# Performance work log

Measured on AMD Instinct MI355X. Metric: run time of the kernel, lower is better.

The kernel has to match this reference:

```python
import jax, jax.numpy as jnp
import numpy as np
from jax import lax

B, S, D = 1, 512, 2048
HK, HV, DK, DV, K = 8, 16, 128, 128, 4
R = HV // HK
KEY_DIM = HK * DK
VAL_DIM = HV * DV
CONV_DIM = 2 * KEY_DIM + VAL_DIM
EPS = 1e-6


def setup_inputs() -> dict:
    key = jax.random.key(0)
    ks = jax.random.split(key, 8)
    hidden_states = jax.random.normal(ks[0], (B, S, D), jnp.float32)
    W_qkvz = jax.random.normal(ks[1], (D, 2 * KEY_DIM + 2 * VAL_DIM), jnp.float32) * 0.02
    W_ba = jax.random.normal(ks[2], (D, 2 * HV), jnp.float32) * 0.02
    conv_w = jax.random.normal(ks[3], (CONV_DIM, 1, K), jnp.float32) * 0.2  # depthwise [C,1,K]
    dt_bias = jnp.ones((HV,), jnp.float32)
    A_log = jnp.log(jax.random.uniform(ks[4], (HV,), jnp.float32, 1e-3, 16.0))
    norm_weight = jnp.ones((DV,), jnp.float32)
    W_out = jax.random.normal(ks[5], (VAL_DIM, D), jnp.float32) * 0.02
    return dict(hidden_states=hidden_states, W_qkvz=W_qkvz, W_ba=W_ba, conv_w=conv_w,
                dt_bias=dt_bias, A_log=A_log, norm_weight=norm_weight, W_out=W_out)


def _l2norm(x):
    return x * lax.rsqrt(jnp.sum(x * x, -1, keepdims=True) + EPS)


def reference(hidden_states, W_qkvz, W_ba, conv_w, dt_bias, A_log, norm_weight, W_out):
    # input projections
    qkvz = hidden_states @ W_qkvz              # [B,S,2*key_dim+2*value_dim]
    ba = hidden_states @ W_ba                  # [B,S,2*HV]
    # _rearrange: split per key-head group
    qkvz = qkvz.reshape(B, S, HK, 2 * DK + 2 * R * DV)
    q = qkvz[..., :DK]                                         # [B,S,HK,DK]
    k = qkvz[..., DK:2 * DK]                                   # [B,S,HK,DK]
    v = qkvz[..., 2 * DK:2 * DK + R * DV].reshape(B, S, HV, DV)
    z = qkvz[..., 2 * DK + R * DV:].reshape(B, S, HV, DV)
    ba = ba.reshape(B, S, HK, 2 * R)
    b = ba[..., :R].reshape(B, S, HV)
    a = ba[..., R:].reshape(B, S, HV)
    # fused causal depthwise conv1d + SiLU over concat(q,k,v)
    mixed = jnp.concatenate([q.reshape(B, S, -1), k.reshape(B, S, -1), v.reshape(B, S, -1)], -1)
    mixed = mixed.transpose(0, 2, 1)           # [B,C,S]
    mixed = lax.conv_general_dilated(mixed, conv_w, (1,), [(K - 1, 0)],
                                     feature_group_count=CONV_DIM,
                                     dimension_numbers=('NCH', 'OIH', 'NCH'))
    mixed = jax.nn.silu(mixed).transpose(0, 2, 1)  # [B,S,C]
    q = mixed[..., :KEY_DIM].reshape(B, S, HK, DK)
    k = mixed[..., KEY_DIM:2 * KEY_DIM].reshape(B, S, HK, DK)
    v = mixed[..., 2 * KEY_DIM:].reshape(B, S, HV, DV)
    # gates
    beta = jax.nn.sigmoid(b)                                   # [B,S,HV]
    g = jnp.exp(-jnp.exp(A_log) * jax.nn.softplus(a + dt_bias))  # per-step decay in (0,1)
    q = _l2norm(q) * (DK ** -0.5)
    k = _l2norm(k)
    q = jnp.repeat(q, R, axis=2)               # GQA expand to HV heads
    k = jnp.repeat(k, R, axis=2)
    # gated delta-rule recurrence over sequence (state per batch/head: [DK,DV])
    def step(Sst, inp):
        qt, kt, vt, gt, bt = inp
        Sst = Sst * gt[..., None, None]
        pred = jnp.einsum('bhk,bhkv->bhv', kt, Sst)
        delta = (vt - pred) * bt[..., None]
        Sst = Sst + jnp.einsum('bhk,bhv->bhkv', kt, delta)
        o = jnp.einsum('bhk,bhkv->bhv', qt, Sst)
        return Sst, o
    xs = (q.transpose(1, 0, 2, 3), k.transpose(1, 0, 2, 3), v.transpose(1, 0, 2, 3),
          g.transpose(1, 0, 2), beta.transpose(1, 0, 2))
    S0 = jnp.zeros((B, HV, DK, DV), jnp.float32)
    _, core = lax.scan(step, S0, xs)           # core: [S,B,HV,DV]
    core = core.transpose(1, 0, 2, 3)          # [B,S,HV,DV]
    # gated RMSNorm per value head, gated by silu(z)
    var = jnp.mean(core * core, -1, keepdims=True)
    normed = core * lax.rsqrt(var + EPS) * norm_weight * jax.nn.silu(z)
    return normed.reshape(B, S, VAL_DIM) @ W_out
```

## Files before the change

kernel.cpp:

```cpp
#include <hip/hip_runtime.h>
#include <hip/hip_bf16.h>
#include <math.h>

#define S_  512
#define D_  2048
#define HK_ 8
#define HV_ 16
#define DK_ 128
#define DV_ 128
#define KEY_DIM_ 1024
#define VAL_DIM_ 2048
#define QKVZ_N  6144
#define EPS_ 1e-6f

typedef __attribute__((ext_vector_type(8))) short short8;
typedef __attribute__((ext_vector_type(4))) float f32x4;
typedef unsigned short ushort_t;
typedef unsigned int uint_t;

__device__ __forceinline__ ushort_t f2bf(float x) {
    uint_t u = __float_as_uint(x);
    return (ushort_t)((u + 0x7FFFu + ((u >> 16) & 1u)) >> 16);
}

__device__ __forceinline__ void gl2lds16(const void* g, void* l) {
    __builtin_amdgcn_global_load_lds((const __attribute__((address_space(1))) uint_t*)g,
                                     (__attribute__((address_space(3))) uint_t*)l, 16, 0, 0);
}
__device__ __forceinline__ void gl2lds4(const void* g, void* l) {
    __builtin_amdgcn_global_load_lds((const __attribute__((address_space(1))) uint_t*)g,
                                     (__attribute__((address_space(3))) uint_t*)l, 4, 0, 0);
}

__global__ __launch_bounds__(256) void convert_bf16(const float* __restrict__ X,
                                                    ushort_t* __restrict__ H, int n4) {
    int i = blockIdx.x * blockDim.x + threadIdx.x;
    if (i >= n4) return;
    float4 v = ((const float4*)X)[i];
    ushort4 h;
    h.x = f2bf(v.x); h.y = f2bf(v.y); h.z = f2bf(v.z); h.w = f2bf(v.w);
    ((ushort4*)H)[i] = h;
}

__global__ __launch_bounds__(256) void transpose_convert(const float* __restrict__ W,
                                                         ushort_t* __restrict__ Th,
                                                         int K, int N) {
    __shared__ float tile[64][65];
    const int kb = blockIdx.y * 64, nb = blockIdx.x * 64;
    const int t = threadIdx.x;
#pragma unroll
    for (int i = 0; i < 4; ++i) {
        int r = (t >> 4) + i * 16;
        int c4 = (t & 15) * 4;
        float4 v = *(const float4*)&W[(size_t)(kb + r) * N + nb + c4];
        tile[r][c4 + 0] = v.x; tile[r][c4 + 1] = v.y;
        tile[r][c4 + 2] = v.z; tile[r][c4 + 3] = v.w;
    }
    __syncthreads();
#pragma unroll
    for (int i = 0; i < 4; ++i) {
        int idx = t + 256 * i;
        int n = idx >> 4;
        int k4 = (idx & 15) * 4;
        ushort4 h;
        h.x = f2bf(tile[k4 + 0][n]); h.y = f2bf(tile[k4 + 1][n]);
        h.z = f2bf(tile[k4 + 2][n]); h.w = f2bf(tile[k4 + 3][n]);
        *(ushort4*)&Th[(size_t)(nb + n) * K + kb + k4] = h;
    }
}

template<int BM, int BN, int WR, int WC>
__global__ __launch_bounds__(256) void gemm_bf16(const ushort_t* __restrict__ A,
                                                 const ushort_t* __restrict__ B,
                                                 float* __restrict__ C,
                                                 int M, int N, int K) {
    constexpr int TM = BM / (16 * WR);
    constexpr int TN = BN / (16 * WC);
    constexpr int AI = (BM / 16) * 2;
    constexpr int BI = (BN / 16) * 2;

    __shared__ __align__(16) ushort_t sA[2][2][BM][32];
    __shared__ __align__(16) ushort_t sB[2][2][BN][32];

    const int t = threadIdx.x;
    const int w = t >> 6, lane = t & 63;
    const int wr = w / WC, wc = w % WC;
    const int lm = lane & 15, quad = lane >> 4;
    const int m0 = blockIdx.y * BM, n0 = blockIdx.x * BN;
    const int lrow = lane >> 2;
    const int lch  = (lane & 3) * 8;

    auto stage = [&](int buf, int k0) {
#pragma unroll
        for (int j = w; j < AI; j += 4) {
            int ks = j & 1, r0 = (j >> 1) * 16;
            gl2lds16(&A[(size_t)(m0 + r0 + lrow) * K + k0 + ks * 32 + lch],
                     &sA[buf][ks][r0][0]);
        }
#pragma unroll
        for (int j = w; j < BI; j += 4) {
            int ks = j & 1, r0 = (j >> 1) * 16;
            gl2lds16(&B[(size_t)(n0 + r0 + lrow) * K + k0 + ks * 32 + lch],
                     &sB[buf][ks][r0][0]);
        }
    };

    f32x4 acc[TM][TN] = {};
    stage(0, 0);
    __syncthreads();

    const int NK = K / 64;
    for (int it = 0; it < NK; ++it) {
        int buf = it & 1;
        if (it + 1 < NK) stage(buf ^ 1, (it + 1) * 64);
#pragma unroll
        for (int ks = 0; ks < 2; ++ks) {
            short8 bf[TN];
#pragma unroll
            for (int ni = 0; ni < TN; ++ni)
                bf[ni] = *(const short8*)&sB[buf][ks][wc * (TN * 16) + ni * 16 + lm][quad * 8];
#pragma unroll
            for (int mi = 0; mi < TM; ++mi) {
                short8 af = *(const short8*)&sA[buf][ks][wr * (TM * 16) + mi * 16 + lm][quad * 8];
#pragma unroll
                for (int ni = 0; ni < TN; ++ni)
                    acc[mi][ni] = __builtin_amdgcn_mfma_f32_16x16x32_bf16(af, bf[ni], acc[mi][ni], 0, 0, 0);
            }
        }
        __syncthreads();
    }

#pragma unroll
    for (int mi = 0; mi < TM; ++mi)
#pragma unroll
        for (int ni = 0; ni < TN; ++ni) {
            int row = m0 + wr * TM * 16 + mi * 16 + quad * 4;
            int col = n0 + wc * TN * 16 + ni * 16 + lm;
#pragma unroll
            for (int r = 0; r < 4; ++r)
                C[(size_t)(row + r) * N + col] = acc[mi][ni][r];
        }
}

__global__ __launch_bounds__(256) void ba_kernel(const float* __restrict__ hid,
                                                 const float* __restrict__ Wba,
                                                 float* __restrict__ ba) {
    const int s = blockIdx.x;
    const int j = threadIdx.x & 31;
    const int kg = threadIdx.x >> 5;
    const float* h = hid + (size_t)s * D_;
    float sum = 0.f;
    const int k0 = kg * 256;
#pragma unroll 8
    for (int k = k0; k < k0 + 256; ++k)
        sum = fmaf(h[k], Wba[(size_t)k * 32 + j], sum);
    __shared__ float red[8][32];
    red[kg][j] = sum;
    __syncthreads();
    if (threadIdx.x < 32) {
        float tot = 0.f;
#pragma unroll
        for (int r = 0; r < 8; ++r) tot += red[r][j];
        ba[s * 32 + j] = tot;
    }
}

__global__ __launch_bounds__(128) void conv_kernel(const float* __restrict__ qkvz,
                                                   const float* __restrict__ conv_w,
                                                   float* __restrict__ qc,
                                                   float* __restrict__ kc,
                                                   float* __restrict__ vc) {
    const int s   = blockIdx.x;
    const int grp = blockIdx.y;
    const int d   = threadIdx.x;

    int col, c;
    if (grp < 8) {
        int hk = grp;
        col = hk * 768 + d;
        c   = hk * 128 + d;
    } else if (grp < 16) {
        int hk = grp - 8;
        col = hk * 768 + 128 + d;
        c   = 1024 + (hk * 128 + d);
    } else {
        int hv = grp - 16;
        col = (hv >> 1) * 768 + 256 + (hv & 1) * 128 + d;
        c   = 2048 + (hv * 128 + d);
    }

    const float w0 = conv_w[c * 4 + 0];
    const float w1 = conv_w[c * 4 + 1];
    const float w2 = conv_w[c * 4 + 2];
    const float w3 = conv_w[c * 4 + 3];

    float x = 0.f;
    if (s - 3 >= 0) x += qkvz[(size_t)(s - 3) * QKVZ_N + col] * w0;
    if (s - 2 >= 0) x += qkvz[(size_t)(s - 2) * QKVZ_N + col] * w1;
    if (s - 1 >= 0) x += qkvz[(size_t)(s - 1) * QKVZ_N + col] * w2;
    x += qkvz[(size_t)s * QKVZ_N + col] * w3;

    x = x / (1.f + expf(-x));

    if (grp < 16) {
        float ss = x * x;
#pragma unroll
        for (int m = 1; m < 64; m <<= 1) ss += __shfl_xor(ss, m);
        __shared__ float red[2];
        int wid = threadIdx.x >> 6;
        if ((threadIdx.x & 63) == 0) red[wid] = ss;
        __syncthreads();
        float tot = red[0] + red[1];
        float scale = rsqrtf(tot + EPS_);
        if (grp < 8) {
            x = x * scale * 0.08838834764831845f;
            qc[((size_t)s * HK_ + grp) * DK_ + d] = x;
        } else {
            x = x * scale;
            kc[((size_t)s * HK_ + (grp - 8)) * DK_ + d] = x;
        }
    } else {
        vc[((size_t)s * HV_ + (grp - 16)) * DV_ + d] = x;
    }
}

__global__ __launch_bounds__(256) void gating_kernel(const float* __restrict__ ba,
                                                     const float* __restrict__ A_log,
                                                     const float* __restrict__ dt_bias,
                                                     float* __restrict__ g,
                                                     float* __restrict__ beta) {
    int id = blockIdx.x * blockDim.x + threadIdx.x;
    if (id >= S_ * HV_) return;
    int s  = id >> 4;
    int hv = id & 15;
    int hk = hv >> 1;
    int r  = hv & 1;
    float b = ba[s * 32 + hk * 4 + r];
    float a = ba[s * 32 + hk * 4 + 2 + r];
    beta[id] = 1.f / (1.f + expf(-b));
    float x  = a + dt_bias[hv];
    float sp = (x > 20.f) ? x : log1pf(expf(x));
    g[id] = expf(-expf(A_log[hv]) * sp);
}

template<int CTRL>
__device__ __forceinline__ float dpp_xor(float x) {
    int v = __builtin_amdgcn_update_dpp(0, __float_as_int(x), CTRL, 0xF, 0xF, true);
    return __int_as_float(v);
}
__device__ __forceinline__ float red32(float x) {
    x += dpp_xor<0xB1>(x);
    x += dpp_xor<0x4E>(x);
    x += dpp_xor<0x141>(x);
    x += dpp_xor<0x140>(x);
    x += __int_as_float(__builtin_amdgcn_ds_swizzle(__float_as_int(x), 0x401F));
    return x;
}

__global__ __launch_bounds__(256) void scal_kernel(const float* __restrict__ kc,
                                                   const float* __restrict__ gbuf,
                                                   const float* __restrict__ bbuf,
                                                   float* __restrict__ scal) {
    const int t  = blockIdx.x;
    const int hk = threadIdx.x >> 5;
    const int s32 = threadIdx.x & 31;

    float c = 0.f;
    if (t > 0) {
        float4 kt = *(const float4*)&kc[((size_t)t * HK_ + hk) * DK_ + s32 * 4];
        float4 kp = *(const float4*)&kc[((size_t)(t - 1) * HK_ + hk) * DK_ + s32 * 4];
        c = fmaf(kt.x, kp.x, 0.f) + kt.y * kp.y + kt.z * kp.z + kt.w * kp.w;
    }
    c = red32(c);

    if (s32 < 2) {
        int h = hk * 2 + s32;
        float gt = gbuf[t * HV_ + h];
        float gp = (t > 0) ? gbuf[(t - 1) * HV_ + h] : 0.f;
        float bt = bbuf[t * HV_ + h];
        float4 o;
        o.x = -gt * c * bt;
        o.y = gt * gp;
        o.z = bt;
        o.w = gt;
        *(float4*)&scal[((size_t)h * S_ + t) * 4] = o;
    }
}

__global__ __launch_bounds__(256) void scan_kernel(const float* __restrict__ qc,
                                                   const float* __restrict__ kc,
                                                   const float* __restrict__ vc,
                                                   const float* __restrict__ scal,
                                                   float* __restrict__ core) {
    const int h = blockIdx.y, v0 = blockIdx.x * 8;
    const int t = threadIdx.x;
    const int lane = t & 63, w = t >> 6;
    const int sub = lane & 31, cw = lane >> 5;
    const int vloc = w * 2 + cw;
    const int v = v0 + vloc;
    const int hk = h >> 1;

    __shared__ __align__(16) float skq[2][32][256];
    __shared__ __align__(16) float sv[2][32][8];
    __shared__ __align__(16) float ssc[2][32][4];

    auto stage = [&](int buf, int c) {
        int t0 = c * 32;
#pragma unroll
        for (int j = 0; j < 8; ++j) {
            int st = w * 8 + j;
            int tt = t0 + st;
            const float* src = (lane < 32)
                ? &kc[((size_t)tt * HK_ + hk) * DK_ + lane * 4]
                : &qc[((size_t)tt * HK_ + hk) * DK_ + (lane - 32) * 4];
            gl2lds16(src, &skq[buf][st][0]);
        }
        {
            int tt = t0 + w * 8 + (lane >> 3);
            gl2lds4(&vc[((size_t)tt * HV_ + h) * DV_ + v0 + (lane & 7)],
                    &sv[buf][w * 8][0]);
        }
        if (w == 0) {
#pragma unroll
            for (int i = 0; i < 2; ++i)
                gl2lds4(&scal[((size_t)h * S_ + t0) * 4 + i * 64 + lane],
                        ((float*)&ssc[buf][0][0]) + i * 64);
        }
    };

    float S0 = 0.f, S1 = 0.f, S2 = 0.f, S3 = 0.f;
    float4 kp = {0.f, 0.f, 0.f, 0.f};
    float4 qp = {0.f, 0.f, 0.f, 0.f};
    float D = 0.f, gprev = 0.f;

    stage(0, 0);
    __syncthreads();

    for (int c = 0; c < 16; ++c) {
        const int buf = c & 1;
        if (c + 1 < 16) stage(buf ^ 1, c + 1);

        float2 kA[3], kB[3], qA[3], qB[3];
        float vr[3];
        float4 sc[3];
        auto rd = [&](int slot, int j) {
            kA[slot] = *(const float2*)&skq[buf][j][sub * 2];
            kB[slot] = *(const float2*)&skq[buf][j][64 + sub * 2];
            qA[slot] = *(const float2*)&skq[buf][j][128 + sub * 2];
            qB[slot] = *(const float2*)&skq[buf][j][192 + sub * 2];
            vr[slot] = sv[buf][j][vloc];
            sc[slot] = *(const float4*)&ssc[buf][j][0];
        };
        rd(0, 0); rd(1, 1);
#pragma unroll
        for (int j = 0; j < 32; ++j) {
            const int sl = j % 3;
            if (j + 2 < 32) rd((j + 2) % 3, j + 2);
            const float4 s4 = sc[sl];
            float u0 = fmaf(kA[sl].x, S0, kA[sl].y * S1);
            float u1 = fmaf(kB[sl].x, S2, kB[sl].y * S3);
            float U = red32(u0 + u1);
            S0 = fmaf(kp.x, D, gprev * S0);
            S1 = fmaf(kp.y, D, gprev * S1);
            S2 = fmaf(kp.z, D, gprev * S2);
            S3 = fmaf(kp.w, D, gprev * S3);
            float o0 = fmaf(qp.x, S0, qp.y * S1);
            float o1 = fmaf(qp.z, S2, qp.w * S3);
            float om = red32(o0 + o1);
            int tg = c * 32 + j;
            if (sub == 0 && tg > 0)
                core[((size_t)(tg - 1) * HV_ + h) * DV_ + v] = om;
            float Q = fmaf(-s4.y, U, vr[sl]) * s4.z;
            D = fmaf(s4.x, D, Q);
            kp = make_float4(kA[sl].x, kA[sl].y, kB[sl].x, kB[sl].y);
            qp = make_float4(qA[sl].x, qA[sl].y, qB[sl].x, qB[sl].y);
            gprev = s4.w;
        }
        __syncthreads();
    }

    S0 = fmaf(kp.x, D, gprev * S0);
    S1 = fmaf(kp.y, D, gprev * S1);
    S2 = fmaf(kp.z, D, gprev * S2);
    S3 = fmaf(kp.w, D, gprev * S3);
    float o0 = fmaf(qp.x, S0, qp.y * S1);
    float o1 = fmaf(qp.z, S2, qp.w * S3);
    float om = red32(o0 + o1);
    if (sub == 0)
        core[((size_t)(S_ - 1) * HV_ + h) * DV_ + v] = om;
}

__global__ __launch_bounds__(128) void normgate_kernel(const float* __restrict__ core,
                                                       const float* __restrict__ qkvz,
                                                       const float* __restrict__ nw,
                                                       ushort_t* __restrict__ nh) {
    const int s  = blockIdx.x;
    const int hv = blockIdx.y;
    const int d  = threadIdx.x;

    float x = core[((size_t)s * HV_ + hv) * DV_ + d];
    float ss = x * x;
#pragma unroll
    for (int m = 1; m < 64; m <<= 1) ss += __shfl_xor(ss, m);
    __shared__ float red[2];
    int wid = threadIdx.x >> 6;
    if ((threadIdx.x & 63) == 0) red[wid] = ss;
    __syncthreads();
    float var = (red[0] + red[1]) * (1.f / 128.f);
    float rs  = rsqrtf(var + EPS_);

    float z  = qkvz[(size_t)s * QKVZ_N + (hv >> 1) * 768 + 512 + (hv & 1) * 128 + d];
    float sz = z / (1.f + expf(-z));

    float y = x * rs * nw[d] * sz;
    nh[(size_t)s * VAL_DIM_ + hv * DV_ + d] = f2bf(y);
}

extern "C" void kernel_launch(void* const* d_in, const int* in_sizes, int n_in,
                              void* d_out, int out_size, void* d_ws, size_t ws_size,
                              hipStream_t stream) {
    const float* hidden  = (const float*)d_in[0];
    const float* W_qkvz  = (const float*)d_in[1];
    const float* W_ba    = (const float*)d_in[2];
    const float* conv_w  = (const float*)d_in[3];
    const float* dt_bias = (const float*)d_in[4];
    const float* A_log   = (const float*)d_in[5];
    const float* norm_w  = (const float*)d_in[6];
    const float* W_out   = (const float*)d_in[7];
    float* out = (float*)d_out;

    char* w = (char*)d_ws;
    auto alloc = [&](size_t bytes) { char* p = w; w += (bytes + 255) & ~(size_t)255; return p; };

    float*    qkvz = (float*)alloc((size_t)S_ * QKVZ_N * 4);
    float*    ba   = (float*)alloc((size_t)S_ * 32 * 4);
    float*    qc   = (float*)alloc((size_t)S_ * KEY_DIM_ * 4);
    float*    kc   = (float*)alloc((size_t)S_ * KEY_DIM_ * 4);
    float*    vc   = (float*)alloc((size_t)S_ * VAL_DIM_ * 4);
    float*    gbuf = (float*)alloc((size_t)S_ * HV_ * 4);
    float*    bbuf = (float*)alloc((size_t)S_ * HV_ * 4);
    float*    scal = (float*)alloc((size_t)HV_ * S_ * 4 * 4);
    float*    core = (float*)alloc((size_t)S_ * VAL_DIM_ * 4);
    ushort_t* hidh = (ushort_t*)alloc((size_t)S_ * D_ * 2);
    ushort_t* nrmh = (ushort_t*)alloc((size_t)S_ * VAL_DIM_ * 2);
    ushort_t* Wqh  = (ushort_t*)alloc((size_t)D_ * QKVZ_N * 2);
    ushort_t* Woh  = (ushort_t*)alloc((size_t)VAL_DIM_ * D_ * 2);

    convert_bf16<<<dim3((S_ * D_ / 4 + 255) / 256), 256, 0, stream>>>(hidden, hidh, S_ * D_ / 4);
    transpose_convert<<<dim3(QKVZ_N / 64, D_ / 64), 256, 0, stream>>>(W_qkvz, Wqh, D_, QKVZ_N);
    transpose_convert<<<dim3(D_ / 64, VAL_DIM_ / 64), 256, 0, stream>>>(W_out, Woh, VAL_DIM_, D_);

    gemm_bf16<64, 128, 1, 4><<<dim3(QKVZ_N / 128, S_ / 64), 256, 0, stream>>>(
        hidh, Wqh, qkvz, S_, QKVZ_N, D_);

    ba_kernel<<<dim3(S_), 256, 0, stream>>>(hidden, W_ba, ba);

    conv_kernel<<<dim3(S_, 32), 128, 0, stream>>>(qkvz, conv_w, qc, kc, vc);

    gating_kernel<<<dim3((S_ * HV_ + 255) / 256), 256, 0, stream>>>(ba, A_log, dt_bias, gbuf, bbuf);

    scal_kernel<<<dim3(S_), 256, 0, stream>>>(kc, gbuf, bbuf, scal);

    scan_kernel<<<dim3(DV_ / 8, HV_), 256, 0, stream>>>(qc, kc, vc, scal, core);

    normgate_kernel<<<dim3(S_, HV_), 128, 0, stream>>>(core, qkvz, norm_w, nrmh);

    gemm_bf16<64, 64, 2, 2><<<dim3(D_ / 64, S_ / 64), 256, 0, stream>>>(
        nrmh, Woh, out, S_, D_, VAL_DIM_);
}
```

Baseline: 292.2 us.

## Shrink scan to one wave per block with 16-lane reductions, fuse gating into scal

The scan kernel is restructured from four waves with a 32-lane split of DK per value column to a single wave where each 16-lane group handles two value columns with 8 keys per lane, using packed float2 math and shorter DPP reductions without a ds_swizzle. The LDS staging is now done by one wave, and the next chunk's first rows are prefetched after the barrier. Separately, the gating kernel is folded into scal_kernel, removing one launch and the g/beta buffers. The trade-off is fewer threads per block and more serial staging work per wave, in exchange for a shorter reduction chain on the sequential critical path.

Result: slower. 299.1 us (+2.4%).

```diff
diff --git a/kernel.cpp b/kernel.cpp
--- a/kernel.cpp
+++ b/kernel.cpp
@@ -15,6 +15,7 @@
 
 typedef __attribute__((ext_vector_type(8))) short short8;
 typedef __attribute__((ext_vector_type(4))) float f32x4;
+typedef __attribute__((ext_vector_type(2))) float v2f;
 typedef unsigned short ushort_t;
 typedef unsigned int uint_t;
 
@@ -224,42 +225,33 @@
     }
 }
 
-__global__ __launch_bounds__(256) void gating_kernel(const float* __restrict__ ba,
-                                                     const float* __restrict__ A_log,
-                                                     const float* __restrict__ dt_bias,
-                                                     float* __restrict__ g,
-                                                     float* __restrict__ beta) {
-    int id = blockIdx.x * blockDim.x + threadIdx.x;
-    if (id >= S_ * HV_) return;
-    int s  = id >> 4;
-    int hv = id & 15;
-    int hk = hv >> 1;
-    int r  = hv & 1;
-    float b = ba[s * 32 + hk * 4 + r];
-    float a = ba[s * 32 + hk * 4 + 2 + r];
-    beta[id] = 1.f / (1.f + expf(-b));
-    float x  = a + dt_bias[hv];
-    float sp = (x > 20.f) ? x : log1pf(expf(x));
-    g[id] = expf(-expf(A_log[hv]) * sp);
-}
-
 template<int CTRL>
 __device__ __forceinline__ float dpp_xor(float x) {
     int v = __builtin_amdgcn_update_dpp(0, __float_as_int(x), CTRL, 0xF, 0xF, true);
     return __int_as_float(v);
 }
-__device__ __forceinline__ float red32(float x) {
+__device__ __forceinline__ float red16(float x) {
     x += dpp_xor<0xB1>(x);
     x += dpp_xor<0x4E>(x);
     x += dpp_xor<0x141>(x);
     x += dpp_xor<0x140>(x);
+    return x;
+}
+__device__ __forceinline__ float red32(float x) {
+    x = red16(x);
     x += __int_as_float(__builtin_amdgcn_ds_swizzle(__float_as_int(x), 0x401F));
     return x;
 }
 
+__device__ __forceinline__ float gate_g(float a, float Aexp) {
+    float sp = (a > 20.f) ? a : log1pf(expf(a));
+    return expf(-Aexp * sp);
+}
+
 __global__ __launch_bounds__(256) void scal_kernel(const float* __restrict__ kc,
-                                                   const float* __restrict__ gbuf,
-                                                   const float* __restrict__ bbuf,
+                                                   const float* __restrict__ ba,
+                                                   const float* __restrict__ A_log,
+                                                   const float* __restrict__ dt_bias,
                                                    float* __restrict__ scal) {
     const int t  = blockIdx.x;
     const int hk = threadIdx.x >> 5;
@@ -269,15 +261,24 @@
     if (t > 0) {
         float4 kt = *(const float4*)&kc[((size_t)t * HK_ + hk) * DK_ + s32 * 4];
         float4 kp = *(const float4*)&kc[((size_t)(t - 1) * HK_ + hk) * DK_ + s32 * 4];
-        c = fmaf(kt.x, kp.x, 0.f) + kt.y * kp.y + kt.z * kp.z + kt.w * kp.w;
+        c = kt.x * kp.x + kt.y * kp.y + kt.z * kp.z + kt.w * kp.w;
     }
     c = red32(c);
 
     if (s32 < 2) {
-        int h = hk * 2 + s32;
-        float gt = gbuf[t * HV_ + h];
-        float gp = (t > 0) ? gbuf[(t - 1) * HV_ + h] : 0.f;
-        float bt = bbuf[t * HV_ + h];
+        int r = s32;
+        int h = hk * 2 + r;
+        float Aexp = expf(A_log[h]);
+        float dtb  = dt_bias[h];
+        float bv = ba[t * 32 + hk * 4 + r];
+        float av = ba[t * 32 + hk * 4 + 2 + r];
+        float bt = 1.f / (1.f + expf(-bv));
+        float gt = gate_g(av + dtb, Aexp);
+        float gp = 0.f;
+        if (t > 0) {
+            float ap = ba[(t - 1) * 32 + hk * 4 + 2 + r];
+            gp = gate_g(ap + dtb, Aexp);
+        }
         float4 o;
         o.x = -gt * c * bt;
         o.y = gt * gp;
@@ -287,17 +288,14 @@
     }
 }
 
-__global__ __launch_bounds__(256) void scan_kernel(const float* __restrict__ qc,
-                                                   const float* __restrict__ kc,
-                                                   const float* __restrict__ vc,
-                                                   const float* __restrict__ scal,
-                                                   float* __restrict__ core) {
+__global__ __launch_bounds__(64) void scan_kernel(const float* __restrict__ qc,
+                                                  const float* __restrict__ kc,
+                                                  const float* __restrict__ vc,
+                                                  const float* __restrict__ scal,
+                                                  float* __restrict__ core) {
     const int h = blockIdx.y, v0 = blockIdx.x * 8;
-    const int t = threadIdx.x;
-    const int lane = t & 63, w = t >> 6;
-    const int sub = lane & 31, cw = lane >> 5;
-    const int vloc = w * 2 + cw;
-    const int v = v0 + vloc;
+    const int lane = threadIdx.x;
+    const int sub = lane & 15, colg = lane >> 4;
     const int hk = h >> 1;
 
     __shared__ __align__(16) float skq[2][32][256];
@@ -305,89 +303,117 @@
     __shared__ __align__(16) float ssc[2][32][4];
 
     auto stage = [&](int buf, int c) {
-        int t0 = c * 32;
-#pragma unroll
-        for (int j = 0; j < 8; ++j) {
-            int st = w * 8 + j;
-            int tt = t0 + st;
+        const int t0 = c * 32;
+        for (int j = 0; j < 32; ++j) {
+            int tt = t0 + j;
             const float* src = (lane < 32)
                 ? &kc[((size_t)tt * HK_ + hk) * DK_ + lane * 4]
                 : &qc[((size_t)tt * HK_ + hk) * DK_ + (lane - 32) * 4];
-            gl2lds16(src, &skq[buf][st][0]);
-        }
-        {
-            int tt = t0 + w * 8 + (lane >> 3);
+            gl2lds16(src, &skq[buf][j][0]);
+        }
+#pragma unroll
+        for (int i = 0; i < 4; ++i) {
+            int tt = t0 + i * 8 + (lane >> 3);
             gl2lds4(&vc[((size_t)tt * HV_ + h) * DV_ + v0 + (lane & 7)],
-                    &sv[buf][w * 8][0]);
-        }
-        if (w == 0) {
-#pragma unroll
-            for (int i = 0; i < 2; ++i)
-                gl2lds4(&scal[((size_t)h * S_ + t0) * 4 + i * 64 + lane],
-                        ((float*)&ssc[buf][0][0]) + i * 64);
-        }
+                    &sv[buf][i * 8][0]);
+        }
+#pragma unroll
+        for (int i = 0; i < 2; ++i)
+            gl2lds4(&scal[((size_t)h * S_ + t0) * 4 + i * 64 + lane],
+                    ((float*)&ssc[buf][0][0]) + i * 64);
     };
 
-    float S0 = 0.f, S1 = 0.f, S2 = 0.f, S3 = 0.f;
-    float4 kp = {0.f, 0.f, 0.f, 0.f};
-    float4 qp = {0.f, 0.f, 0.f, 0.f};
-    float D = 0.f, gprev = 0.f;
+    v2f  S0[4] = {}, S1[4] = {};
+    v2f  kS[4][4] = {}, qS[4][4] = {};
+    float vS[4][2] = {};
+    float4 scS[4] = {};
+    float D0 = 0.f, D1 = 0.f;
 
     stage(0, 0);
     __syncthreads();
+
+    auto rd = [&](int slot, int buf, int j) {
+#pragma unroll
+        for (int i = 0; i < 4; ++i) {
+            kS[slot][i] = *(const v2f*)&skq[buf][j][sub * 8 + i * 2];
+            qS[slot][i] = *(const v2f*)&skq[buf][j][128 + sub * 8 + i * 2];
+        }
+        vS[slot][0] = sv[buf][j][colg];
+        vS[slot][1] = sv[buf][j][colg + 4];
+        scS[slot] = *(const float4*)&ssc[buf][j][0];
+    };
+
+    rd(0, 0, 0);
+    rd(1, 0, 1);
 
     for (int c = 0; c < 16; ++c) {
         const int buf = c & 1;
         if (c + 1 < 16) stage(buf ^ 1, c + 1);
 
-        float2 kA[3], kB[3], qA[3], qB[3];
-        float vr[3];
-        float4 sc[3];
-        auto rd = [&](int slot, int j) {
-            kA[slot] = *(const float2*)&skq[buf][j][sub * 2];
-            kB[slot] = *(const float2*)&skq[buf][j][64 + sub * 2];
-            qA[slot] = *(const float2*)&skq[buf][j][128 + sub * 2];
-            qB[slot] = *(const float2*)&skq[buf][j][192 + sub * 2];
-            vr[slot] = sv[buf][j][vloc];
-            sc[slot] = *(const float4*)&ssc[buf][j][0];
-        };
-        rd(0, 0); rd(1, 1);
 #pragma unroll
         for (int j = 0; j < 32; ++j) {
-            const int sl = j % 3;
-            if (j + 2 < 32) rd((j + 2) % 3, j + 2);
-            const float4 s4 = sc[sl];
-            float u0 = fmaf(kA[sl].x, S0, kA[sl].y * S1);
-            float u1 = fmaf(kB[sl].x, S2, kB[sl].y * S3);
-            float U = red32(u0 + u1);
-            S0 = fmaf(kp.x, D, gprev * S0);
-            S1 = fmaf(kp.y, D, gprev * S1);
-            S2 = fmaf(kp.z, D, gprev * S2);
-            S3 = fmaf(kp.w, D, gprev * S3);
-            float o0 = fmaf(qp.x, S0, qp.y * S1);
-            float o1 = fmaf(qp.z, S2, qp.w * S3);
-            float om = red32(o0 + o1);
-            int tg = c * 32 + j;
-            if (sub == 0 && tg > 0)
-                core[((size_t)(tg - 1) * HV_ + h) * DV_ + v] = om;
-            float Q = fmaf(-s4.y, U, vr[sl]) * s4.z;
-            D = fmaf(s4.x, D, Q);
-            kp = make_float4(kA[sl].x, kA[sl].y, kB[sl].x, kB[sl].y);
-            qp = make_float4(qA[sl].x, qA[sl].y, qB[sl].x, qB[sl].y);
-            gprev = s4.w;
+            const int cur = j & 3, prv = (j + 3) & 3;
+            if (j < 30) rd((j + 2) & 3, buf, j + 2);
+
+            v2f ua = kS[cur][0] * S0[0] + kS[cur][1] * S0[1]
+                   + kS[cur][2] * S0[2] + kS[cur][3] * S0[3];
+            v2f ub = kS[cur][0] * S1[0] + kS[cur][1] * S1[1]
+                   + kS[cur][2] * S1[2] + kS[cur][3] * S1[3];
+            float Ua = red16(ua.x + ua.y);
+            float Ub = red16(ub.x + ub.y);
+
+            const float gp = scS[prv].w;
+            const v2f gp2 = {gp, gp};
+            const v2f Da2 = {D0, D0}, Db2 = {D1, D1};
+#pragma unroll
+            for (int i = 0; i < 4; ++i) {
+                S0[i] = kS[prv][i] * Da2 + gp2 * S0[i];
+                S1[i] = kS[prv][i] * Db2 + gp2 * S1[i];
+            }
+
+            v2f oa = qS[prv][0] * S0[0] + qS[prv][1] * S0[1]
+                   + qS[prv][2] * S0[2] + qS[prv][3] * S0[3];
+            v2f ob = qS[prv][0] * S1[0] + qS[prv][1] * S1[1]
+                   + qS[prv][2] * S1[2] + qS[prv][3] * S1[3];
+            float Oa = red16(oa.x + oa.y);
+            float Ob = red16(ob.x + ob.y);
+            const int tg = c * 32 + j;
+            if (sub == 0 && tg > 0) {
+                core[((size_t)(tg - 1) * HV_ + h) * DV_ + v0 + colg] = Oa;
+                core[((size_t)(tg - 1) * HV_ + h) * DV_ + v0 + colg + 4] = Ob;
+            }
+
+            const float P = scS[cur].x, W1 = scS[cur].y, be = scS[cur].z;
+            D0 = fmaf(P, D0, (vS[cur][0] - W1 * Ua) * be);
+            D1 = fmaf(P, D1, (vS[cur][1] - W1 * Ub) * be);
         }
         __syncthreads();
-    }
-
-    S0 = fmaf(kp.x, D, gprev * S0);
-    S1 = fmaf(kp.y, D, gprev * S1);
-    S2 = fmaf(kp.z, D, gprev * S2);
-    S3 = fmaf(kp.w, D, gprev * S3);
-    float o0 = fmaf(qp.x, S0, qp.y * S1);
-    float o1 = fmaf(qp.z, S2, qp.w * S3);
-    float om = red32(o0 + o1);
-    if (sub == 0)
-        core[((size_t)(S_ - 1) * HV_ + h) * DV_ + v] = om;
+        if (c + 1 < 16) {
+            rd(0, buf ^ 1, 0);
+            rd(1, buf ^ 1, 1);
+        }
+    }
+
+    {
+        const float gp = scS[3].w;
+        const v2f gp2 = {gp, gp};
+        const v2f Da2 = {D0, D0}, Db2 = {D1, D1};
+#pragma unroll
+        for (int i = 0; i < 4; ++i) {
+            S0[i] = kS[3][i] * Da2 + gp2 * S0[i];
+            S1[i] = kS[3][i] * Db2 + gp2 * S1[i];
+        }
+        v2f oa = qS[3][0] * S0[0] + qS[3][1] * S0[1]
+               + qS[3][2] * S0[2] + qS[3][3] * S0[3];
+        v2f ob = qS[3][0] * S1[0] + qS[3][1] * S1[1]
+               + qS[3][2] * S1[2] + qS[3][3] * S1[3];
+        float Oa = red16(oa.x + oa.y);
+        float Ob = red16(ob.x + ob.y);
+        if (sub == 0) {
+            core[((size_t)(S_ - 1) * HV_ + h) * DV_ + v0 + colg] = Oa;
+            core[((size_t)(S_ - 1) * HV_ + h) * DV_ + v0 + colg + 4] = Ob;
+        }
+    }
 }
 
 __global__ __launch_bounds__(128) void normgate_kernel(const float* __restrict__ core,
@@ -437,8 +463,6 @@
     float*    qc   = (float*)alloc((size_t)S_ * KEY_DIM_ * 4);
     float*    kc   = (float*)alloc((size_t)S_ * KEY_DIM_ * 4);
     float*    vc   = (float*)alloc((size_t)S_ * VAL_DIM_ * 4);
-    float*    gbuf = (float*)alloc((size_t)S_ * HV_ * 4);
-    float*    bbuf = (float*)alloc((size_t)S_ * HV_ * 4);
     float*    scal = (float*)alloc((size_t)HV_ * S_ * 4 * 4);
     float*    core = (float*)alloc((size_t)S_ * VAL_DIM_ * 4);
     ushort_t* hidh = (ushort_t*)alloc((size_t)S_ * D_ * 2);
@@ -457,11 +481,9 @@
 
     conv_kernel<<<dim3(S_, 32), 128, 0, stream>>>(qkvz, conv_w, qc, kc, vc);
 
-    gating_kernel<<<dim3((S_ * HV_ + 255) / 256), 256, 0, stream>>>(ba, A_log, dt_bias, gbuf, bbuf);
-
-    scal_kernel<<<dim3(S_), 256, 0, stream>>>(kc, gbuf, bbuf, scal);
-
-    scan_kernel<<<dim3(DV_ / 8, HV_), 256, 0, stream>>>(qc, kc, vc, scal, core);
+    scal_kernel<<<dim3(S_), 256, 0, stream>>>(kc, ba, A_log, dt_bias, scal);
+
+    scan_kernel<<<dim3(DV_ / 8, HV_), 64, 0, stream>>>(qc, kc, vc, scal, core);
 
     normgate_kernel<<<dim3(S_, HV_), 128, 0, stream>>>(core, qkvz, norm_w, nrmh);
 
```
